# Performance work log

Hardware: AMD Instinct MI355X
Metric: run time of the kernel (lower is better)

## Reference

```python
import jax, jax.numpy as jnp
import numpy as np
import math

H = 12   # num_attention_heads
DH = 64  # attention_head_size
HID = H * DH  # 768


def setup_inputs() -> dict:
    key = jax.random.key(0)
    ks = jax.random.split(key, 16)
    B, S = 2, 128
    inp = {
        'hidden_states': jax.random.normal(ks[0], (B, S, HID), jnp.float32),
        'attention_mask': jnp.zeros((B, 1, 1, S), jnp.float32),
        'inference_path': jax.random.normal(ks[1], (B, S, S, HID), jnp.float32),
        'span_mask': jax.random.uniform(ks[2], (B, 1, S, S), jnp.float32),
    }
    sc = 1.0 / math.sqrt(HID)
    # weights stored as [in, out]; y = x @ W + b
    inp['Wq'] = jax.random.normal(ks[3], (HID, HID), jnp.float32) * sc
    inp['bq'] = jnp.zeros((HID,), jnp.float32)
    inp['Wk'] = jax.random.normal(ks[4], (HID, HID), jnp.float32) * sc
    inp['bk'] = jnp.zeros((HID,), jnp.float32)
    inp['Wv'] = jax.random.normal(ks[5], (HID, HID), jnp.float32) * sc
    inp['bv'] = jnp.zeros((HID,), jnp.float32)
    inp['Wpv'] = jax.random.normal(ks[6], (HID, DH), jnp.float32) * sc
    inp['bpv'] = jnp.zeros((DH,), jnp.float32)
    inp['Wip'] = jax.random.normal(ks[7], (HID, 2 * HID), jnp.float32) * sc
    inp['Wmlp'] = jax.random.normal(ks[8], (HID + DH, HID), jnp.float32) * sc
    inp['bmlp'] = jnp.zeros((HID,), jnp.float32)
    return inp


def reference(hidden_states, attention_mask, inference_path, span_mask,
              Wq, bq, Wk, bk, Wv, bv, Wpv, bpv, Wip, Wmlp, bmlp):
    B, S, _ = hidden_states.shape
    # projections
    q = (hidden_states @ Wq + bq).reshape(B, S, H, DH).transpose(0, 2, 1, 3)  # [B,H,S,Dh]
    k = (hidden_states @ Wk + bk).reshape(B, S, H, DH).transpose(0, 2, 1, 3)
    v = (hidden_states @ Wv + bv).reshape(B, S, H, DH).transpose(0, 2, 1, 3)
    # parse value path: [B,1,S,Dh]
    pv = (hidden_states @ Wpv + bpv).reshape(B, S, 1, DH).transpose(0, 2, 1, 3)
    parse_ctx = jnp.matmul(span_mask, pv)              # [B,1,S,Dh]
    parse_ctx = parse_ctx.transpose(0, 2, 1, 3)        # [B,S,1,Dh]
    # relative inference-path bias: raw view (matches torch .view semantics)
    ip = inference_path @ Wip                           # [B,S,S,2*HID]
    ra, rb = jnp.split(ip, 2, axis=-1)                  # each [B,S,S,HID]
    ra = ra.reshape(B, H, S, S, DH)
    rb = rb.reshape(B, H, S, S, DH)
    qe = q[:, :, :, None, :] + ra                       # [B,H,S,S,Dh]
    ke = k[:, :, None, :, :] + rb                       # [B,H,S,S,Dh]
    scores = jnp.einsum('bhqkd,bhqkd->bhqk', qe, ke)
    scores = scores / math.sqrt(DH) + attention_mask
    probs = jax.nn.softmax(scores, axis=-1)             # dropout is identity in eval
    ctx = jnp.matmul(probs, v)                          # [B,H,S,Dh]
    ctx = ctx.transpose(0, 2, 1, 3)                     # [B,S,H,Dh]
    ctx = jnp.concatenate([ctx, parse_ctx], axis=-2)    # [B,S,H+1,Dh]
    ctx = ctx.reshape(B, S, HID + DH)
    return ctx @ Wmlp + bmlp                            # [B,S,HID]
```

## Files before the change

kernel.cpp:

```cpp
#include <hip/hip_runtime.h>
#include <hip/hip_bf16.h>


typedef __attribute__((ext_vector_type(8))) __bf16 bf16x8;
typedef __attribute__((ext_vector_type(16))) float f32x16;

#define QKV_OFF   0u
#define ARENA_OFF 2424832u
#define SC_OFF    4784128u
#define CTX_OFF   6356992u

__global__ __launch_bounds__(256)
void prep_kernel(const float* __restrict__ Wip, __bf16* __restrict__ arena) {
  const int l = threadIdx.x & 63;
  const int f = blockIdx.x * 4 + (threadIdx.x >> 6);
  const int n32 = f / 48, k16 = f - n32 * 48;
  const float* src = Wip + (size_t)(k16 * 16 + (l >> 5) * 8) * 1536 + n32 * 32 + (l & 31);
  union { __bf16 h[8]; uint4 u; } pk;
#pragma unroll
  for (int j = 0; j < 8; j++) pk.h[j] = (__bf16)src[(size_t)j * 1536];
  ((uint4*)arena)[(size_t)f * 64 + l] = pk.u;
}

__global__ __launch_bounds__(64)
void proj_kernel(const float* __restrict__ hs,
                 const float* __restrict__ Wq, const float* __restrict__ bq,
                 const float* __restrict__ Wk, const float* __restrict__ bk,
                 const float* __restrict__ Wv, const float* __restrict__ bv,
                 const float* __restrict__ Wpv, const float* __restrict__ bpv,
                 float* __restrict__ qkv) {
  const int n0 = blockIdx.x * 32;
  const int m0 = blockIdx.y * 32;
  const float* W; const float* bias; int noff, ldw;
  if (n0 < 768)       { W = Wq;  bias = bq;  noff = n0;        ldw = 768; }
  else if (n0 < 1536) { W = Wk;  bias = bk;  noff = n0 - 768;  ldw = 768; }
  else if (n0 < 2304) { W = Wv;  bias = bv;  noff = n0 - 1536; ldw = 768; }
  else                { W = Wpv; bias = bpv; noff = n0 - 2304; ldw = 64;  }
  const int l = threadIdx.x;
  const int rsel = l & 31, ksel = l >> 5;
  f32x16 acc;
#pragma unroll
  for (int z = 0; z < 16; z++) acc[z] = 0.f;

#pragma unroll 4
  for (int k16 = 0; k16 < 48; k16++) {
    const float* ap = hs + (size_t)(m0 + rsel) * 768 + k16 * 16 + ksel * 8;
    float4 a0 = *(const float4*)ap;
    float4 a1 = *(const float4*)(ap + 4);
    union { __bf16 h[8]; bf16x8 v; } pa;
    pa.h[0] = (__bf16)a0.x; pa.h[1] = (__bf16)a0.y; pa.h[2] = (__bf16)a0.z; pa.h[3] = (__bf16)a0.w;
    pa.h[4] = (__bf16)a1.x; pa.h[5] = (__bf16)a1.y; pa.h[6] = (__bf16)a1.z; pa.h[7] = (__bf16)a1.w;
    const float* bp = W + (size_t)(k16 * 16 + ksel * 8) * ldw + noff + rsel;
    union { __bf16 h[8]; bf16x8 v; } pb;
#pragma unroll
    for (int j = 0; j < 8; j++) pb.h[j] = (__bf16)bp[(size_t)j * ldw];
    acc = __builtin_amdgcn_mfma_f32_32x32x16_bf16(pa.v, pb.v, acc, 0, 0, 0);
  }
#pragma unroll
  for (int reg = 0; reg < 16; reg++) {
    int row = (reg & 3) + ((reg >> 2) << 3) + (ksel << 2);
    qkv[(size_t)(m0 + row) * 2368 + n0 + rsel] = acc[reg] + bias[noff + rsel];
  }
}

extern __shared__ char smem_raw[];

__global__ __launch_bounds__(512, 2)
void score_kernel(const float* __restrict__ infp,
                  const __bf16* __restrict__ arena,
                  const float* __restrict__ qkv,
                  float* __restrict__ scores) {
  char* Abase = smem_raw;
  float* lds_sc = (float*)(smem_raw + 99840);
  const int tid = threadIdx.x;
  const int lane = tid & 63;
  const int ml = lane & 31;
  const int kh = lane >> 5;
  const int wv = tid >> 6;
  const int wc = wv & 3;
  const int wd = wv >> 2;
  const int blk = blockIdx.x;
  const int b = blk >> 8;
  const int r0 = (blk & 255) << 6;

  for (int z = tid; z < 768; z += 512) lds_sc[z] = 0.f;

  {
    const float4* A4 = (const float4*)(infp + (size_t)(b * 16384 + r0) * 768);
#pragma unroll
    for (int p = 0; p < 12; p++) {
      int idx = p * 512 + tid;
      int m = (int)(((unsigned)idx * 10923u) >> 20);
      int g = idx - m * 96;
      float4 v0 = A4[m * 192 + g * 2];
      float4 v1 = A4[m * 192 + g * 2 + 1];
      union { __bf16 h[8]; uint4 u; } pk;
      pk.h[0] = (__bf16)v0.x; pk.h[1] = (__bf16)v0.y;
      pk.h[2] = (__bf16)v0.z; pk.h[3] = (__bf16)v0.w;
      pk.h[4] = (__bf16)v1.x; pk.h[5] = (__bf16)v1.y;
      pk.h[6] = (__bf16)v1.z; pk.h[7] = (__bf16)v1.w;
      int F = (m >> 5) * 48 + (g >> 1);
      int slot = (m & 31) + ((g & 1) << 5);
      *(uint4*)(Abase + ((F * 65 + slot) << 4)) = pk.u;
    }
  }
  __syncthreads();

  const size_t lane_off = (size_t)(lane << 4);
  const uint4* BA = (const uint4*)arena;
  uint4 B0[8], B1[8];
  bf16x8 Af[8];
  f32x16 acc_ra[2], acc_rb[2];

  auto loadB = [&](uint4* dst, int c, int kc) {
    const uint4* pa = BA + (size_t)(((2 * c + wd) * 48 + kc * 4) * 64) + lane;
#pragma unroll
    for (int ks = 0; ks < 4; ks++) {
      dst[ks * 2]     = pa[ks * 64];
      dst[ks * 2 + 1] = pa[ks * 64 + 73728];
    }
  };
  auto loadA = [&](int kc) {
#pragma unroll
    for (int mt = 0; mt < 2; mt++)
#pragma unroll
      for (int ks = 0; ks < 4; ks++)
        Af[mt * 4 + ks] = *(const bf16x8*)(Abase + (((mt * 48 + kc * 4 + ks) * 65) << 4) + lane_off);
  };
  auto mfma_step = [&](uint4* Bb) {
#pragma unroll
    for (int ks = 0; ks < 4; ks++) {
      bf16x8 bra = *(bf16x8*)&Bb[ks * 2];
      bf16x8 brb = *(bf16x8*)&Bb[ks * 2 + 1];
#pragma unroll
      for (int mt = 0; mt < 2; mt++) {
        acc_ra[mt] = __builtin_amdgcn_mfma_f32_32x32x16_bf16(Af[mt * 4 + ks], bra, acc_ra[mt], 0, 0, 0);
        acc_rb[mt] = __builtin_amdgcn_mfma_f32_32x32x16_bf16(Af[mt * 4 + ks], brb, acc_rb[mt], 0, 0, 0);
      }
    }
  };
  auto epilogue = [&](int c) {
    int d = wd * 32 + ml;
#pragma unroll
    for (int mt = 0; mt < 2; mt++) {
      float qv[16], kv[16];
#pragma unroll
      for (int reg = 0; reg < 16; reg++) {
        int row = mt * 32 + (reg & 3) + ((reg >> 2) << 3) + (kh << 2);
        int t = 12 * (r0 + row) + c;
        int hh = t >> 14;
        int ii = (t >> 7) & 127;
        int jj = t & 127;
        qv[reg] = qkv[(size_t)((b << 7) + ii) * 2368 + (hh << 6) + d];
        kv[reg] = qkv[(size_t)((b << 7) + jj) * 2368 + 768 + (hh << 6) + d];
      }
#pragma unroll
      for (int reg = 0; reg < 16; reg++) {
        int row = mt * 32 + (reg & 3) + ((reg >> 2) << 3) + (kh << 2);
        float p = (qv[reg] + acc_ra[mt][reg]) * (kv[reg] + acc_rb[mt][reg]);
        p += __shfl_xor(p, 16);
        p += __shfl_xor(p, 8);
        p += __shfl_xor(p, 4);
        p += __shfl_xor(p, 2);
        p += __shfl_xor(p, 1);
        if (ml == 0) atomicAdd(&lds_sc[row * 12 + c], p);
      }
    }
#pragma unroll
    for (int mt = 0; mt < 2; mt++)
#pragma unroll
      for (int z = 0; z < 16; z++) { acc_ra[mt][z] = 0.f; acc_rb[mt][z] = 0.f; }
  };

#pragma unroll
  for (int mt = 0; mt < 2; mt++)
#pragma unroll
    for (int z = 0; z < 16; z++) { acc_ra[mt][z] = 0.f; acc_rb[mt][z] = 0.f; }

  loadB(B0, wc, 0);
  int kc = 0, c = wc;
#pragma unroll 1
  for (int ith = 0; ith < 18; ith++) {
    {
      int kcn = kc + 1, cn = c;
      if (kcn == 12) { kcn = 0; cn = c + 4; }
      loadA(kc);
      loadB(B1, cn, kcn);
      __builtin_amdgcn_sched_barrier(0);
      mfma_step(B0);
      kc = kcn; c = cn;
    }
    {
      int kcn = kc + 1, cn = c;
      if (kcn == 12) { kcn = 0; cn = c + 4; }
      loadA(kc);
      if (ith < 17) loadB(B0, cn, kcn);
      __builtin_amdgcn_sched_barrier(0);
      mfma_step(B1);
      if (kc == 11) epilogue(c);
      kc = kcn; c = cn;
    }
  }

  __syncthreads();
  for (int z = tid; z < 768; z += 512) {
    int row = z / 12;
    int cc = z - row * 12;
    int t = 12 * (r0 + row) + cc;
    int hh = t >> 14;
    int ii = (t >> 7) & 127;
    int jj = t & 127;
    scores[(size_t)((b * 12 + hh) * 128 + ii) * 128 + jj] = lds_sc[z];
  }
}

__global__ __launch_bounds__(256)
void attn_kernel(const float* __restrict__ scores, const float* __restrict__ qkv,
                 const float* __restrict__ mask, const float* __restrict__ span,
                 float* __restrict__ ctx) {
  const int i = blockIdx.x;
  const int b = blockIdx.y;
  const int tid = threadIdx.x;
  const int l = tid & 63;
  const int wvi = tid >> 6;
  __shared__ float w[13][132];
  for (int r = wvi; r < 13; r += 4) {
    if (r < 12) {
      const float* sp = scores + (size_t)((b * 12 + r) * 128 + i) * 128;
      float s0 = sp[l] * 0.125f + mask[b * 128 + l];
      float s1 = sp[l + 64] * 0.125f + mask[b * 128 + l + 64];
      float mx = fmaxf(s0, s1);
#pragma unroll
      for (int o = 32; o; o >>= 1) mx = fmaxf(mx, __shfl_xor(mx, o));
      float e0 = __expf(s0 - mx), e1 = __expf(s1 - mx);
      float sm = e0 + e1;
#pragma unroll
      for (int o = 32; o; o >>= 1) sm += __shfl_xor(sm, o);
      float inv = 1.f / sm;
      w[r][l] = e0 * inv;
      w[r][l + 64] = e1 * inv;
    } else {
      const float* sp = span + (size_t)(b * 128 + i) * 128;
      w[12][l] = sp[l];
      w[12][l + 64] = sp[l + 64];
    }
  }
  __syncthreads();
  for (int o = tid; o < 832; o += 256) {
    int h = o >> 6, d = o & 63;
    const float* vp = qkv + (size_t)(b * 128) * 2368 + (h < 12 ? 1536 + h * 64 : 2304) + d;
    float acc = 0.f;
#pragma unroll 8
    for (int j = 0; j < 128; j++) acc += w[h][j] * vp[(size_t)j * 2368];
    ctx[(size_t)(b * 128 + i) * 832 + o] = acc;
  }
}

__global__ __launch_bounds__(64)
void out_kernel(const float* __restrict__ ctxb, const float* __restrict__ Wmlp,
                const float* __restrict__ bmlp, float* __restrict__ out) {
  const int n0 = blockIdx.x * 32;
  const int m0 = blockIdx.y * 32;
  const int l = threadIdx.x;
  const int rsel = l & 31, ksel = l >> 5;
  f32x16 acc;
#pragma unroll
  for (int z = 0; z < 16; z++) acc[z] = 0.f;

#pragma unroll 4
  for (int k16 = 0; k16 < 52; k16++) {
    const float* ap = ctxb + (size_t)(m0 + rsel) * 832 + k16 * 16 + ksel * 8;
    float4 a0 = *(const float4*)ap;
    float4 a1 = *(const float4*)(ap + 4);
    union { __bf16 h[8]; bf16x8 v; } pa;
    pa.h[0] = (__bf16)a0.x; pa.h[1] = (__bf16)a0.y; pa.h[2] = (__bf16)a0.z; pa.h[3] = (__bf16)a0.w;
    pa.h[4] = (__bf16)a1.x; pa.h[5] = (__bf16)a1.y; pa.h[6] = (__bf16)a1.z; pa.h[7] = (__bf16)a1.w;
    const float* bp = Wmlp + (size_t)(k16 * 16 + ksel * 8) * 768 + n0 + rsel;
    union { __bf16 h[8]; bf16x8 v; } pb;
#pragma unroll
    for (int j = 0; j < 8; j++) pb.h[j] = (__bf16)bp[(size_t)j * 768];
    acc = __builtin_amdgcn_mfma_f32_32x32x16_bf16(pa.v, pb.v, acc, 0, 0, 0);
  }
#pragma unroll
  for (int reg = 0; reg < 16; reg++) {
    int row = (reg & 3) + ((reg >> 2) << 3) + (ksel << 2);
    out[(size_t)(m0 + row) * 768 + n0 + rsel] = acc[reg] + bmlp[n0 + rsel];
  }
}

extern "C" void kernel_launch(void* const* d_in, const int* in_sizes, int n_in,
                              void* d_out, int out_size, void* d_ws, size_t ws_size,
                              hipStream_t stream) {
  const float* hs   = (const float*)d_in[0];
  const float* mask = (const float*)d_in[1];
  const float* infp = (const float*)d_in[2];
  const float* span = (const float*)d_in[3];
  const float* Wq   = (const float*)d_in[4];
  const float* bq   = (const float*)d_in[5];
  const float* Wk   = (const float*)d_in[6];
  const float* bk   = (const float*)d_in[7];
  const float* Wv   = (const float*)d_in[8];
  const float* bv   = (const float*)d_in[9];
  const float* Wpv  = (const float*)d_in[10];
  const float* bpv  = (const float*)d_in[11];
  const float* Wip  = (const float*)d_in[12];
  const float* Wmlp = (const float*)d_in[13];
  const float* bmlp = (const float*)d_in[14];
  float* out = (float*)d_out;

  char* ws = (char*)d_ws;
  float*  qkv    = (float*)(ws + QKV_OFF);
  __bf16* arena  = (__bf16*)(ws + ARENA_OFF);
  float*  scores = (float*)(ws + SC_OFF);
  float*  ctx    = (float*)(ws + CTX_OFF);

  prep_kernel<<<dim3(576), 256, 0, stream>>>(Wip, arena);
  proj_kernel<<<dim3(74, 8), 64, 0, stream>>>(hs, Wq, bq, Wk, bk, Wv, bv, Wpv, bpv, qkv);
  score_kernel<<<dim3(512), 512, 102912, stream>>>(infp, arena, qkv, scores);
  attn_kernel<<<dim3(128, 2), 256, 0, stream>>>(scores, qkv, mask, span, ctx);
  out_kernel<<<dim3(24, 8), 64, 0, stream>>>(ctx, Wmlp, bmlp, out);
}
```

Measured before the change: 370.4 us.

## Transpose score MFMA so rows map to lanes; store QKV in bf16

The score kernel now puts the inference-path rows on the MFMA N dimension and all 64 head-dim columns on M. Each lane then holds a full row's partial dot product, so the per-row shuffle tree and LDS atomics are replaced by one cross-half shuffle and a direct global store. QKV projections are written in bf16 to halve epilogue and attention V traffic. The Q/K/V weights are prepacked into MFMA layout in the prep kernel, and the projection loop prefetches its next A/B operands. This lowers QKV precision and doubles per-wave accumulator and weight registers, which may pressure occupancy.

```diff
diff --git a/kernel.cpp b/kernel.cpp
--- a/kernel.cpp
+++ b/kernel.cpp
@@ -3,63 +3,83 @@
 
 
 typedef __attribute__((ext_vector_type(8))) __bf16 bf16x8;
+typedef __attribute__((ext_vector_type(4))) __bf16 bf16x4;
 typedef __attribute__((ext_vector_type(16))) float f32x16;
 
-#define QKV_OFF   0u
-#define ARENA_OFF 2424832u
-#define SC_OFF    4784128u
-#define CTX_OFF   6356992u
+#define ARENA_OFF 1212416u
+#define X_OFF     3571712u
+#define CTX_OFF   5144576u
 
 __global__ __launch_bounds__(256)
-void prep_kernel(const float* __restrict__ Wip, __bf16* __restrict__ arena) {
+void prep_kernel(const float* __restrict__ Wip, const float* __restrict__ Wq,
+                 const float* __restrict__ Wk, const float* __restrict__ Wv,
+                 const float* __restrict__ Wpv,
+                 __bf16* __restrict__ arena, __bf16* __restrict__ arena2) {
   const int l = threadIdx.x & 63;
   const int f = blockIdx.x * 4 + (threadIdx.x >> 6);
-  const int n32 = f / 48, k16 = f - n32 * 48;
-  const float* src = Wip + (size_t)(k16 * 16 + (l >> 5) * 8) * 1536 + n32 * 32 + (l & 31);
+  const float* src; int ldw, k16, colbase;
+  if (f < 2304) {
+    int n32 = f / 48; k16 = f - n32 * 48;
+    src = Wip; ldw = 1536; colbase = n32 * 32;
+  } else {
+    int f2 = f - 2304;
+    int n32 = f2 / 48; k16 = f2 - n32 * 48;
+    int col = n32 * 32;
+    if (col < 768)       { src = Wq;  ldw = 768; colbase = col; }
+    else if (col < 1536) { src = Wk;  ldw = 768; colbase = col - 768; }
+    else if (col < 2304) { src = Wv;  ldw = 768; colbase = col - 1536; }
+    else                 { src = Wpv; ldw = 64;  colbase = col - 2304; }
+  }
+  const float* p = src + (size_t)(k16 * 16 + (l >> 5) * 8) * ldw + colbase + (l & 31);
   union { __bf16 h[8]; uint4 u; } pk;
 #pragma unroll
-  for (int j = 0; j < 8; j++) pk.h[j] = (__bf16)src[(size_t)j * 1536];
-  ((uint4*)arena)[(size_t)f * 64 + l] = pk.u;
+  for (int j = 0; j < 8; j++) pk.h[j] = (__bf16)p[(size_t)j * ldw];
+  if (f < 2304) ((uint4*)arena)[(size_t)f * 64 + l] = pk.u;
+  else          ((uint4*)arena2)[(size_t)(f - 2304) * 64 + l] = pk.u;
 }
 
 __global__ __launch_bounds__(64)
-void proj_kernel(const float* __restrict__ hs,
-                 const float* __restrict__ Wq, const float* __restrict__ bq,
-                 const float* __restrict__ Wk, const float* __restrict__ bk,
-                 const float* __restrict__ Wv, const float* __restrict__ bv,
-                 const float* __restrict__ Wpv, const float* __restrict__ bpv,
-                 float* __restrict__ qkv) {
+void proj_kernel(const float* __restrict__ hs, const __bf16* __restrict__ arena2,
+                 const float* __restrict__ bq, const float* __restrict__ bk,
+                 const float* __restrict__ bv, const float* __restrict__ bpv,
+                 __bf16* __restrict__ qkvb) {
   const int n0 = blockIdx.x * 32;
   const int m0 = blockIdx.y * 32;
-  const float* W; const float* bias; int noff, ldw;
-  if (n0 < 768)       { W = Wq;  bias = bq;  noff = n0;        ldw = 768; }
-  else if (n0 < 1536) { W = Wk;  bias = bk;  noff = n0 - 768;  ldw = 768; }
-  else if (n0 < 2304) { W = Wv;  bias = bv;  noff = n0 - 1536; ldw = 768; }
-  else                { W = Wpv; bias = bpv; noff = n0 - 2304; ldw = 64;  }
   const int l = threadIdx.x;
   const int rsel = l & 31, ksel = l >> 5;
+  const float* bias; int noff;
+  if (n0 < 768)       { bias = bq;  noff = n0; }
+  else if (n0 < 1536) { bias = bk;  noff = n0 - 768; }
+  else if (n0 < 2304) { bias = bv;  noff = n0 - 1536; }
+  else                { bias = bpv; noff = n0 - 2304; }
+  const uint4* BF = (const uint4*)arena2 + (size_t)blockIdx.x * 48 * 64 + l;
+  const float* abase = hs + (size_t)(m0 + rsel) * 768 + ksel * 8;
   f32x16 acc;
 #pragma unroll
   for (int z = 0; z < 16; z++) acc[z] = 0.f;
 
-#pragma unroll 4
+  float4 a0 = *(const float4*)abase;
+  float4 a1 = *(const float4*)(abase + 4);
+  uint4 bcur = BF[0];
+#pragma unroll 1
   for (int k16 = 0; k16 < 48; k16++) {
-    const float* ap = hs + (size_t)(m0 + rsel) * 768 + k16 * 16 + ksel * 8;
-    float4 a0 = *(const float4*)ap;
-    float4 a1 = *(const float4*)(ap + 4);
+    float4 na0, na1; uint4 bn;
+    if (k16 < 47) {
+      const float* np = abase + (k16 + 1) * 16;
+      na0 = *(const float4*)np;
+      na1 = *(const float4*)(np + 4);
+      bn = BF[(k16 + 1) * 64];
+    }
     union { __bf16 h[8]; bf16x8 v; } pa;
     pa.h[0] = (__bf16)a0.x; pa.h[1] = (__bf16)a0.y; pa.h[2] = (__bf16)a0.z; pa.h[3] = (__bf16)a0.w;
     pa.h[4] = (__bf16)a1.x; pa.h[5] = (__bf16)a1.y; pa.h[6] = (__bf16)a1.z; pa.h[7] = (__bf16)a1.w;
-    const float* bp = W + (size_t)(k16 * 16 + ksel * 8) * ldw + noff + rsel;
-    union { __bf16 h[8]; bf16x8 v; } pb;
-#pragma unroll
-    for (int j = 0; j < 8; j++) pb.h[j] = (__bf16)bp[(size_t)j * ldw];
-    acc = __builtin_amdgcn_mfma_f32_32x32x16_bf16(pa.v, pb.v, acc, 0, 0, 0);
+    acc = __builtin_amdgcn_mfma_f32_32x32x16_bf16(pa.v, *(bf16x8*)&bcur, acc, 0, 0, 0);
+    a0 = na0; a1 = na1; bcur = bn;
   }
 #pragma unroll
   for (int reg = 0; reg < 16; reg++) {
     int row = (reg & 3) + ((reg >> 2) << 3) + (ksel << 2);
-    qkv[(size_t)(m0 + row) * 2368 + n0 + rsel] = acc[reg] + bias[noff + rsel];
+    qkvb[(size_t)(m0 + row) * 2368 + n0 + rsel] = (__bf16)(acc[reg] + bias[noff + rsel]);
   }
 }
 
@@ -68,22 +88,19 @@
 __global__ __launch_bounds__(512, 2)
 void score_kernel(const float* __restrict__ infp,
                   const __bf16* __restrict__ arena,
-                  const float* __restrict__ qkv,
+                  const __bf16* __restrict__ qkvb,
                   float* __restrict__ scores) {
   char* Abase = smem_raw;
-  float* lds_sc = (float*)(smem_raw + 99840);
   const int tid = threadIdx.x;
   const int lane = tid & 63;
-  const int ml = lane & 31;
+  const int rl = lane & 31;
   const int kh = lane >> 5;
   const int wv = tid >> 6;
   const int wc = wv & 3;
-  const int wd = wv >> 2;
+  const int ws = wv >> 2;
   const int blk = blockIdx.x;
   const int b = blk >> 8;
   const int r0 = (blk & 255) << 6;
-
-  for (int z = tid; z < 768; z += 512) lds_sc[z] = 0.f;
 
   {
     const float4* A4 = (const float4*)(infp + (size_t)(b * 16384 + r0) * 768);
@@ -108,114 +125,105 @@
 
   const size_t lane_off = (size_t)(lane << 4);
   const uint4* BA = (const uint4*)arena;
-  uint4 B0[8], B1[8];
-  bf16x8 Af[8];
-  f32x16 acc_ra[2], acc_rb[2];
-
-  auto loadB = [&](uint4* dst, int c, int kc) {
-    const uint4* pa = BA + (size_t)(((2 * c + wd) * 48 + kc * 4) * 64) + lane;
+  uint4 W0[16], W1[16];
+  bf16x8 ip0[4], ip1[4];
+  f32x16 acc[4];
+
+  auto loadW = [&](uint4* dst, int c, int kc) {
+    const uint4* pa = BA + (size_t)((2 * c * 48 + kc * 4) * 64) + lane;
 #pragma unroll
     for (int ks = 0; ks < 4; ks++) {
-      dst[ks * 2]     = pa[ks * 64];
-      dst[ks * 2 + 1] = pa[ks * 64 + 73728];
+      dst[ks * 4 + 0] = pa[ks * 64];
+      dst[ks * 4 + 1] = pa[ks * 64 + 3072];
+      dst[ks * 4 + 2] = pa[ks * 64 + 73728];
+      dst[ks * 4 + 3] = pa[ks * 64 + 76800];
     }
   };
-  auto loadA = [&](int kc) {
-#pragma unroll
-    for (int mt = 0; mt < 2; mt++)
-#pragma unroll
-      for (int ks = 0; ks < 4; ks++)
-        Af[mt * 4 + ks] = *(const bf16x8*)(Abase + (((mt * 48 + kc * 4 + ks) * 65) << 4) + lane_off);
+  auto loadIP = [&](bf16x8* dst, int kc) {
+#pragma unroll
+    for (int ks = 0; ks < 4; ks++)
+      dst[ks] = *(const bf16x8*)(Abase + (((ws * 48 + kc * 4 + ks) * 65) << 4) + lane_off);
   };
-  auto mfma_step = [&](uint4* Bb) {
+  auto step = [&](uint4* W, bf16x8* ip) {
 #pragma unroll
     for (int ks = 0; ks < 4; ks++) {
-      bf16x8 bra = *(bf16x8*)&Bb[ks * 2];
-      bf16x8 brb = *(bf16x8*)&Bb[ks * 2 + 1];
-#pragma unroll
-      for (int mt = 0; mt < 2; mt++) {
-        acc_ra[mt] = __builtin_amdgcn_mfma_f32_32x32x16_bf16(Af[mt * 4 + ks], bra, acc_ra[mt], 0, 0, 0);
-        acc_rb[mt] = __builtin_amdgcn_mfma_f32_32x32x16_bf16(Af[mt * 4 + ks], brb, acc_rb[mt], 0, 0, 0);
-      }
+      acc[0] = __builtin_amdgcn_mfma_f32_32x32x16_bf16(*(bf16x8*)&W[ks * 4 + 0], ip[ks], acc[0], 0, 0, 0);
+      acc[2] = __builtin_amdgcn_mfma_f32_32x32x16_bf16(*(bf16x8*)&W[ks * 4 + 1], ip[ks], acc[2], 0, 0, 0);
+      acc[1] = __builtin_amdgcn_mfma_f32_32x32x16_bf16(*(bf16x8*)&W[ks * 4 + 2], ip[ks], acc[1], 0, 0, 0);
+      acc[3] = __builtin_amdgcn_mfma_f32_32x32x16_bf16(*(bf16x8*)&W[ks * 4 + 3], ip[ks], acc[3], 0, 0, 0);
     }
   };
   auto epilogue = [&](int c) {
-    int d = wd * 32 + ml;
-#pragma unroll
-    for (int mt = 0; mt < 2; mt++) {
-      float qv[16], kv[16];
-#pragma unroll
-      for (int reg = 0; reg < 16; reg++) {
-        int row = mt * 32 + (reg & 3) + ((reg >> 2) << 3) + (kh << 2);
-        int t = 12 * (r0 + row) + c;
-        int hh = t >> 14;
-        int ii = (t >> 7) & 127;
-        int jj = t & 127;
-        qv[reg] = qkv[(size_t)((b << 7) + ii) * 2368 + (hh << 6) + d];
-        kv[reg] = qkv[(size_t)((b << 7) + jj) * 2368 + 768 + (hh << 6) + d];
+    int row_g = r0 + ws * 32 + rl;
+    int t = 12 * row_g + c;
+    int hh = t >> 14;
+    int ii = (t >> 7) & 127;
+    int jj = t & 127;
+    const __bf16* qb = qkvb + (size_t)((b << 7) + ii) * 2368 + (hh << 6) + 4 * kh;
+    const __bf16* kb = qkvb + (size_t)((b << 7) + jj) * 2368 + 768 + (hh << 6) + 4 * kh;
+    bf16x4 qv[8], kv[8];
+#pragma unroll
+    for (int g = 0; g < 4; g++) {
+      qv[g]     = *(const bf16x4*)(qb + g * 8);
+      qv[g + 4] = *(const bf16x4*)(qb + 32 + g * 8);
+      kv[g]     = *(const bf16x4*)(kb + g * 8);
+      kv[g + 4] = *(const bf16x4*)(kb + 32 + g * 8);
+    }
+    float p = 0.f;
+#pragma unroll
+    for (int g = 0; g < 4; g++)
+#pragma unroll
+      for (int e = 0; e < 4; e++) {
+        p += ((float)qv[g][e] + acc[0][g * 4 + e]) * ((float)kv[g][e] + acc[1][g * 4 + e]);
+        p += ((float)qv[g + 4][e] + acc[2][g * 4 + e]) * ((float)kv[g + 4][e] + acc[3][g * 4 + e]);
       }
-#pragma unroll
-      for (int reg = 0; reg < 16; reg++) {
-        int row = mt * 32 + (reg & 3) + ((reg >> 2) << 3) + (kh << 2);
-        float p = (qv[reg] + acc_ra[mt][reg]) * (kv[reg] + acc_rb[mt][reg]);
-        p += __shfl_xor(p, 16);
-        p += __shfl_xor(p, 8);
-        p += __shfl_xor(p, 4);
-        p += __shfl_xor(p, 2);
-        p += __shfl_xor(p, 1);
-        if (ml == 0) atomicAdd(&lds_sc[row * 12 + c], p);
-      }
-    }
-#pragma unroll
-    for (int mt = 0; mt < 2; mt++)
-#pragma unroll
-      for (int z = 0; z < 16; z++) { acc_ra[mt][z] = 0.f; acc_rb[mt][z] = 0.f; }
+    p += __shfl_xor(p, 32);
+    if (kh == 0)
+      scores[(size_t)((b * 12 + hh) * 128 + ii) * 128 + jj] = p;
+#pragma unroll
+    for (int q = 0; q < 4; q++)
+#pragma unroll
+      for (int z = 0; z < 16; z++) acc[q][z] = 0.f;
   };
 
 #pragma unroll
-  for (int mt = 0; mt < 2; mt++)
-#pragma unroll
-    for (int z = 0; z < 16; z++) { acc_ra[mt][z] = 0.f; acc_rb[mt][z] = 0.f; }
-
-  loadB(B0, wc, 0);
+  for (int q = 0; q < 4; q++)
+#pragma unroll
+    for (int z = 0; z < 16; z++) acc[q][z] = 0.f;
+
+  loadW(W0, wc, 0);
+  loadIP(ip0, 0);
   int kc = 0, c = wc;
 #pragma unroll 1
   for (int ith = 0; ith < 18; ith++) {
     {
       int kcn = kc + 1, cn = c;
-      if (kcn == 12) { kcn = 0; cn = c + 4; }
-      loadA(kc);
-      loadB(B1, cn, kcn);
+      loadIP(ip1, kcn);
+      loadW(W1, cn, kcn);
       __builtin_amdgcn_sched_barrier(0);
-      mfma_step(B0);
+      step(W0, ip0);
       kc = kcn; c = cn;
     }
     {
       int kcn = kc + 1, cn = c;
       if (kcn == 12) { kcn = 0; cn = c + 4; }
-      loadA(kc);
-      if (ith < 17) loadB(B0, cn, kcn);
-      __builtin_amdgcn_sched_barrier(0);
-      mfma_step(B1);
-      if (kc == 11) epilogue(c);
+      if (kc != 11) {
+        loadIP(ip0, kcn);
+        loadW(W0, cn, kcn);
+        __builtin_amdgcn_sched_barrier(0);
+        step(W1, ip1);
+      } else {
+        step(W1, ip1);
+        epilogue(c);
+        if (ith < 17) { loadIP(ip0, 0); loadW(W0, cn, 0); }
+      }
       kc = kcn; c = cn;
     }
   }
-
-  __syncthreads();
-  for (int z = tid; z < 768; z += 512) {
-    int row = z / 12;
-    int cc = z - row * 12;
-    int t = 12 * (r0 + row) + cc;
-    int hh = t >> 14;
-    int ii = (t >> 7) & 127;
-    int jj = t & 127;
-    scores[(size_t)((b * 12 + hh) * 128 + ii) * 128 + jj] = lds_sc[z];
-  }
 }
 
 __global__ __launch_bounds__(256)
-void attn_kernel(const float* __restrict__ scores, const float* __restrict__ qkv,
+void attn_kernel(const float* __restrict__ scores, const __bf16* __restrict__ qkvb,
                  const float* __restrict__ mask, const float* __restrict__ span,
                  float* __restrict__ ctx) {
   const int i = blockIdx.x;
@@ -248,10 +256,10 @@
   __syncthreads();
   for (int o = tid; o < 832; o += 256) {
     int h = o >> 6, d = o & 63;
-    const float* vp = qkv + (size_t)(b * 128) * 2368 + (h < 12 ? 1536 + h * 64 : 2304) + d;
+    const __bf16* vp = qkvb + (size_t)(b * 128) * 2368 + (h < 12 ? 1536 + h * 64 : 2304) + d;
     float acc = 0.f;
 #pragma unroll 8
-    for (int j = 0; j < 128; j++) acc += w[h][j] * vp[(size_t)j * 2368];
+    for (int j = 0; j < 128; j++) acc += w[h][j] * (float)vp[(size_t)j * 2368];
     ctx[(size_t)(b * 128 + i) * 832 + o] = acc;
   }
 }
@@ -309,14 +317,15 @@
   float* out = (float*)d_out;
 
   char* ws = (char*)d_ws;
-  float*  qkv    = (float*)(ws + QKV_OFF);
+  __bf16* qkvb   = (__bf16*)(ws);
   __bf16* arena  = (__bf16*)(ws + ARENA_OFF);
-  float*  scores = (float*)(ws + SC_OFF);
+  __bf16* arena2 = (__bf16*)(ws + X_OFF);
+  float*  scores = (float*)(ws + X_OFF);
   float*  ctx    = (float*)(ws + CTX_OFF);
 
-  prep_kernel<<<dim3(576), 256, 0, stream>>>(Wip, arena);
-  proj_kernel<<<dim3(74, 8), 64, 0, stream>>>(hs, Wq, bq, Wk, bk, Wv, bv, Wpv, bpv, qkv);
-  score_kernel<<<dim3(512), 512, 102912, stream>>>(infp, arena, qkv, scores);
-  attn_kernel<<<dim3(128, 2), 256, 0, stream>>>(scores, qkv, mask, span, ctx);
+  prep_kernel<<<dim3(1464), 256, 0, stream>>>(Wip, Wq, Wk, Wv, Wpv, arena, arena2);
+  proj_kernel<<<dim3(74, 8), 64, 0, stream>>>(hs, arena2, bq, bk, bv, bpv, qkvb);
+  score_kernel<<<dim3(512), 512, 99840, stream>>>(infp, arena, qkvb, scores);
+  attn_kernel<<<dim3(128, 2), 256, 0, stream>>>(scores, qkvb, mask, span, ctx);
   out_kernel<<<dim3(24, 8), 64, 0, stream>>>(ctx, Wmlp, bmlp, out);
 }
```

Result: slower. 891.8 us (+140.7%).
